# Performance work log

Measured on AMD Instinct MI355X. Metric: run time of the kernel, lower is better.

## Reference

```python
import jax, jax.numpy as jnp
from jax import lax
import numpy as np

B, N, C = 8, 10647, 80          # batch, total anchors (416px YOLOv3), COCO classes
MAX_BOXES = 100                  # yolo_max_boxes (per class and total, like combined NMS)
IOU_TH = 0.5
SCORE_TH = 0.3


def setup_inputs() -> dict:
    key = jax.random.key(0)
    k1, k2, k3, k4 = jax.random.split(key, 4)
    # valid corner-format boxes (x1,y1,x2,y2) in [0,1]
    xy = jax.random.uniform(k1, (B, N, 2), dtype=jnp.float32) * 0.9
    wh = jax.random.uniform(k2, (B, N, 2), dtype=jnp.float32) * 0.1 + 0.01
    boxes = jnp.concatenate([xy, xy + wh], axis=-1)
    confidence = jax.random.uniform(k3, (B, N, 1), dtype=jnp.float32)
    class_probs = jax.random.uniform(k4, (B, N, C), dtype=jnp.float32)
    return {"boxes": boxes, "confidence": confidence, "class_probs": class_probs}


def _iou_one_vs_all(box, boxes):
    # box [4], boxes [N,4], corner format
    x1 = jnp.maximum(box[0], boxes[:, 0])
    y1 = jnp.maximum(box[1], boxes[:, 1])
    x2 = jnp.minimum(box[2], boxes[:, 2])
    y2 = jnp.minimum(box[3], boxes[:, 3])
    inter = jnp.maximum(x2 - x1, 0.0) * jnp.maximum(y2 - y1, 0.0)
    area_a = (box[2] - box[0]) * (box[3] - box[1])
    area_b = (boxes[:, 2] - boxes[:, 0]) * (boxes[:, 3] - boxes[:, 1])
    return inter / (area_a + area_b - inter + 1e-9)


def _nms_one_class(scores_c, bxs):
    # scores_c [N], bxs [N,4]: greedy NMS, returns MAX_BOXES candidates
    s0 = jnp.where(scores_c > SCORE_TH, scores_c, -1.0)

    def step(cur, _):
        i = jnp.argmax(cur)
        sc = cur[i]
        b = bxs[i]
        ious = _iou_one_vs_all(b, bxs)
        nxt = jnp.where(ious > IOU_TH, -1.0, cur).at[i].set(-1.0)
        valid = sc > 0.0
        return nxt, (jnp.where(valid, sc, 0.0),
                     jnp.where(valid, b, jnp.zeros(4, b.dtype)),
                     valid)

    _, (ss, bb, vv) = lax.scan(step, s0, None, length=MAX_BOXES)
    return bb, ss, vv  # [M,4], [M], [M]


def reference(boxes, confidence, class_probs):
    # scores per class: objectness * class prob  -> [B, C, N]
    scores = jnp.transpose(confidence * class_probs, (0, 2, 1))
    per_class = jax.vmap(jax.vmap(_nms_one_class, in_axes=(0, None)), in_axes=(0, 0))
    cb, cs, cv = per_class(scores, boxes)           # [B,C,M,4], [B,C,M], [B,C,M]

    flat_s = cs.reshape(B, -1)                       # [B, C*M]
    flat_b = cb.reshape(B, -1, 4)
    flat_v = cv.reshape(B, -1)
    cls_ids = jnp.broadcast_to(
        jnp.arange(C, dtype=jnp.float32)[:, None], (C, MAX_BOXES)).reshape(-1)

    top_s, top_i = lax.top_k(flat_s, MAX_BOXES)      # merge across classes
    sel_b = jnp.take_along_axis(flat_b, top_i[..., None], axis=1)
    sel_v = jnp.take_along_axis(flat_v, top_i, axis=1)
    sel_c = jnp.where(sel_v, cls_ids[top_i], 0.0)
    sel_s = jnp.where(sel_v, top_s, 0.0)
    num_valid = jnp.sum(sel_v, axis=1).astype(jnp.int32)
    return sel_b, sel_s, sel_c, num_valid
```

## Files before the change

kernel.cpp:

```cpp
#include <hip/hip_runtime.h>

#define Bn 8
#define Nn 10647
#define Cn 80
#define MAXB 100
#define SCORE_TH 0.3f
#define BGUESS 0.82f
#define IOU_THR 0.5f
#define NBIN 4096
#define NB2 1024
#define SORT_CAP 256
#define TARGET 160
#define CH 128
#define PCAP 16
#define TOT (Cn * MAXB)
#define TOTQ (TOT / 4)
#define MREG 8

__device__ __forceinline__ int score_bin(float s) {
    int v = (int)(__float_as_uint(s) >> 12) - 0x3E999 + 1;
    v = v < 1 ? 1 : v;
    return v > NBIN - 1 ? NBIN - 1 : v;
}
__device__ __forceinline__ int score_bin2(float s) {
    int v = (int)(__float_as_uint(s) >> 14) - 0xFA66 + 1;
    v = v < 1 ? 1 : v;
    return v > NB2 - 1 ? NB2 - 1 : v;
}

__device__ __forceinline__ bool iou_gt(const float4 s, const float4 c) {
    float x1 = fmaxf(s.x, c.x), y1 = fmaxf(s.y, c.y);
    float x2 = fminf(s.z, c.z), y2 = fminf(s.w, c.w);
    float inter = fmaxf(x2 - x1, 0.0f) * fmaxf(y2 - y1, 0.0f);
    float aS = (s.z - s.x) * (s.w - s.y);
    float aC = (c.z - c.x) * (c.w - c.y);
    return inter > IOU_THR * (aS + aC - inter + 1e-9f);
}

__global__ __launch_bounds__(256) void collect(
    const float* __restrict__ conf, const float* __restrict__ cp,
    int* __restrict__ pcnt, unsigned long long* __restrict__ glist)
{
    __shared__ float lconf[88];
    __shared__ int cnt3[Cn];
    __shared__ int cnt9[Cn];
    int tid = threadIdx.x;
    int b = blockIdx.x / CH;
    int ch = blockIdx.x % CH;

    for (int i = tid; i < Cn; i += 256) { cnt3[i] = 0; cnt9[i] = 0; }

    const int totq = Nn * 20;
    const int per = (totq + CH - 1) / CH;
    int q0 = ch * per;
    int q1 = q0 + per; if (q1 > totq) q1 = totq;
    int n0 = q0 / 20;
    int nspan = (q1 - 1) / 20 - n0 + 1;

    const float* confB = conf + b * Nn;
    for (int i = tid; i < nspan; i += 256) lconf[i] = confB[n0 + i];
    __syncthreads();

    const float4* cp4 = (const float4*)(cp + (size_t)b * Nn * Cn);

    for (int q = q0 + tid; q < q1; q += 256) {
        float4 v = cp4[q];
        int n = q / 20;
        int c0 = (q % 20) * 4;
        float cf = lconf[n - n0];
        float sv[4] = {v.x, v.y, v.z, v.w};
#pragma unroll
        for (int e = 0; e < 4; ++e) {
            float s = cf * sv[e];
            if (s > SCORE_TH) {
                atomicAdd(&cnt3[c0 + e], 1);
                if (s > BGUESS) {
                    int pos = atomicAdd(&cnt9[c0 + e], 1);
                    if (pos < PCAP)
                        glist[((size_t)(b * Cn + c0 + e) * CH + ch) * PCAP + pos] =
                            ((unsigned long long)__float_as_uint(s) << 32) |
                            (unsigned)(Nn - 1 - n);
                }
            }
        }
    }
    __syncthreads();
    for (int c = tid; c < Cn; c += 256)
        pcnt[(size_t)(b * Cn + c) * CH + ch] = (cnt3[c] & 0xFFFF) | (cnt9[c] << 16);
}

__global__ __launch_bounds__(512) void nms_class(
    const float* __restrict__ boxes, const float* __restrict__ conf,
    const float* __restrict__ cp,
    const int* __restrict__ pcnt, const unsigned long long* __restrict__ glist,
    float* __restrict__ wss, float4* __restrict__ wsb)
{
    __shared__ unsigned long long keys[SORT_CAP];
    __shared__ float ssc[SORT_CAP];
    __shared__ float4 sbx[SORT_CAP];
    __shared__ float4 bxu[SORT_CAP];
    __shared__ unsigned short cj[SORT_CAP][3];
    __shared__ int ncA[SORT_CAP];
    __shared__ unsigned char selv[SORT_CAP], resv[SORT_CAP], confl[SORT_CAP];
    __shared__ int rpart[SORT_CAP];
    __shared__ int chc[CH], chOff[CH], pscan[CH];
    __shared__ int hist2[NB2];
    __shared__ int suf[257];
    __shared__ int wtot[4];
    __shared__ int sh_tot, sh_ovf, sh_hard, sh_B, sh_M, sh_nsel;

    int tid = threadIdx.x;
    int lane = tid & 63, wv = tid >> 6;
    int bc = blockIdx.x;
    int b = bc / Cn, c = bc % Cn;

    if (tid == 0) { sh_tot = 0; sh_ovf = 0; sh_hard = 0; sh_nsel = 0; }
    for (int i = tid; i < SORT_CAP; i += 512) ncA[i] = 0;
    __syncthreads();

    if (tid < CH) {
        int p = pcnt[(size_t)(b * Cn + c) * CH + tid];
        int c9 = p >> 16;
        if (c9 > PCAP) { atomicOr(&sh_ovf, 1); c9 = PCAP; }
        chc[tid] = c9;
        atomicAdd(&sh_tot, p & 0xFFFF);
        int incl = c9;
#pragma unroll
        for (int off = 1; off < 64; off <<= 1) {
            int o = __shfl_up(incl, off);
            if (lane >= off) incl += o;
        }
        pscan[tid] = incl;
    }
    float* ws_s = wss + bc * MAXB;
    float4* ws_b = wsb + bc * MAXB;
    for (int i = tid; i < MAXB; i += 512) ws_s[i] = 0.0f;
    __syncthreads();
    if (tid < CH) {
        int base = (tid >= 64) ? pscan[63] : 0;
        chOff[tid] = base + pscan[tid] - chc[tid];
    }
    __syncthreads();

    int cnt = pscan[63] + pscan[127];
    int tot = sh_tot;
    bool fast = (!sh_ovf) && (cnt <= SORT_CAP);
    int M = fast ? cnt : 0;

    if (fast) {
        const unsigned long long* slotC = glist + (size_t)(b * Cn + c) * CH * PCAP;
        for (int i = tid; i < CH * PCAP; i += 512) {
            int ch = i >> 4, j = i & (PCAP - 1);
            if (j < chc[ch]) keys[chOff[ch] + j] = slotC[i];
        }
    }
    __syncthreads();

    const float4* boxesB = (const float4*)boxes + (size_t)b * Nn;
    int cand = tid & 255, half = tid >> 8;
    bool act = (cand < M);

    unsigned long long k0 = 0;
    float4 b0 = make_float4(0, 0, 0, 0);
    if (act) k0 = keys[cand];
    if (act && half == 0) b0 = boxesB[Nn - 1 - (int)(k0 & 0xffffffffu)];
    int r0 = 0;
    if (act) {
#pragma unroll 4
        for (int j = half; j < M; j += 2) r0 += (keys[j] > k0) ? 1 : 0;
    }
    if (act && half == 1) rpart[cand] = r0;
    __syncthreads();
    if (act && half == 0) {
        int rank = r0 + rpart[cand];
        ssc[rank] = __uint_as_float((unsigned)(k0 >> 32));
        sbx[rank] = b0;
    }
    __syncthreads();

    if (act) {
        float4 tb = sbx[cand];
#pragma unroll 2
        for (int j = half; j < cand; j += 2) {
            float4 bj = sbx[j];
            if (iou_gt(bj, tb)) {
                int s = atomicAdd(&ncA[cand], 1);
                if (s < 3) cj[cand][s] = (unsigned short)j;
            }
        }
    }
    __syncthreads();
    if (tid < SORT_CAP && tid < M && ncA[tid] > 3) atomicOr(&sh_hard, 1);
    __syncthreads();

    if (!sh_hard) {
        bool mysel = false, myres = false;
        if (tid < SORT_CAP) {
            myres = (tid < M) ? (ncA[tid] == 0) : true;
            mysel = (tid < M) && myres;
            selv[tid] = mysel ? 1 : 0;
            resv[tid] = myres ? 1 : 0;
        }
        __syncthreads();
        while (true) {
            bool upd = false, upd_sel = false;
            if (tid < SORT_CAP && tid < M && !myres) {
                int nc = ncA[tid];
                bool allr = true, anysel = false;
                for (int k = 0; k < nc; ++k) {
                    int j = cj[tid][k];
                    allr = allr && (resv[j] != 0);
                    anysel = anysel || (selv[j] != 0);
                }
                if (allr) { upd = true; upd_sel = !anysel; }
            }
            __syncthreads();
            if (upd) {
                myres = true; mysel = upd_sel;
                selv[tid] = mysel ? 1 : 0; resv[tid] = 1;
            }
            int unres = __syncthreads_count((tid < SORT_CAP && tid < M && !myres) ? 1 : 0);
            if (unres == 0) break;
        }
        int v = (tid < SORT_CAP && mysel) ? 1 : 0;
        int incl = v;
        if (tid < SORT_CAP) {
#pragma unroll
            for (int off = 1; off < 64; off <<= 1) {
                int o = __shfl_up(incl, off);
                if (lane >= off) incl += o;
            }
            if (lane == 63) wtot[wv] = incl;
        }
        __syncthreads();
        if (tid < SORT_CAP) {
            int base = 0;
            for (int w = 0; w < wv; ++w) base += wtot[w];
            int pos = base + incl - v;
            if (v && pos < MAXB) { ws_s[pos] = ssc[tid]; ws_b[pos] = sbx[tid]; }
            if (tid == 0) sh_nsel = wtot[0] + wtot[1] + wtot[2] + wtot[3];
        }
        __syncthreads();
    } else {
        if (tid < SORT_CAP) confl[tid] = (tid < M && ncA[tid] > 0) ? 1 : 0;
        __syncthreads();
        if (tid < 64) {
            float4 sA = make_float4(0, 0, 0, 0), sB = make_float4(0, 0, 0, 0);
            int nsel = 0;
            for (int w0 = 0; w0 < M && nsel < MAXB; w0 += 64) {
                int wlim = M - w0; if (wlim > 64) wlim = 64;
                bool cfl = (tid < wlim) ? (confl[w0 + tid] != 0) : false;
                unsigned long long cmask = __ballot(cfl);
                int pos = 0;
                while (pos < wlim && nsel < MAXB) {
                    if (!((cmask >> pos) & 1ULL)) {
                        unsigned long long rest = cmask >> pos;
                        int run = rest ? (__ffsll(rest) - 1) : (wlim - pos);
                        if (run > wlim - pos) run = wlim - pos;
                        int avail = MAXB - nsel; if (run > avail) run = avail;
                        int d = (tid - (nsel & 63)) & 63;
                        if (d < run) {
                            int s = nsel + d;
                            int ci = w0 + pos + d;
                            float4 bx = sbx[ci];
                            if (s < 64) sA = bx; else sB = bx;
                            ws_s[s] = ssc[ci]; ws_b[s] = bx;
                        }
                        nsel += run; pos += run;
                    } else {
                        int ci = w0 + pos;
                        float4 bx = sbx[ci];
                        bool sup = (tid < nsel) && iou_gt(sA, bx);
                        if (tid + 64 < nsel) sup = sup || iou_gt(sB, bx);
                        if (__ballot(sup) == 0ULL) {
                            if (tid == (nsel & 63)) { if (nsel < 64) sA = bx; else sB = bx; }
                            if (tid == 0) { ws_s[nsel] = ssc[ci]; ws_b[nsel] = bx; }
                            ++nsel;
                        }
                        ++pos;
                    }
                }
            }
            if (tid == 0) sh_nsel = nsel;
        }
        __syncthreads();
    }

    bool needSlow = (!fast) || !((sh_nsel >= MAXB) || (cnt == tot));
    if (!needSlow) return;

    for (int i = tid; i < MAXB; i += 512) ws_s[i] = 0.0f;
    for (int i = tid; i < NB2; i += 512) hist2[i] = 0;
    if (tid == 0) sh_nsel = 0;
    __syncthreads();

    const float* confB = conf + b * Nn;
    const float* cpB = cp + (size_t)b * Nn * Cn + c;
    for (int n = tid; n < Nn; n += 512) {
        float s = confB[n] * cpB[(size_t)n * Cn];
        if (s > SCORE_TH) atomicAdd(&hist2[score_bin2(s)], 1);
    }
    __syncthreads();

    float4 sA = make_float4(0, 0, 0, 0), sB = make_float4(0, 0, 0, 0);
    int hi = NB2;
    int round = 0;

    while (true) {
        if (tid < 256) {
            int ps = 0;
#pragma unroll
            for (int u = 0; u < 4; ++u) ps += hist2[tid * 4 + u];
            int p = ps;
#pragma unroll
            for (int off = 1; off < 64; off <<= 1) {
                int v = __shfl_down(p, off);
                if (lane + off < 64) p += v;
            }
            if (lane == 0) wtot[wv] = p;
        }
        __syncthreads();
        if (tid < 256) {
            int add = 0;
            for (int w2 = wv + 1; w2 < 4; ++w2) add += wtot[w2];
            suf[tid] = ((tid < 256) ? 0 : 0) + add + ((lane < 64) ? 0 : 0);
        }
        __syncthreads();
        if (tid < 256) {
            int ps = 0;
#pragma unroll
            for (int u = 0; u < 4; ++u) ps += hist2[tid * 4 + u];
            int p = ps;
#pragma unroll
            for (int off = 1; off < 64; off <<= 1) {
                int v = __shfl_down(p, off);
                if (lane + off < 64) p += v;
            }
            int add = 0;
            for (int w2 = wv + 1; w2 < 4; ++w2) add += wtot[w2];
            suf[tid] = p + add;
            if (tid == 0) suf[256] = 0;
        }
        __syncthreads();

        int total = suf[0];
        if (total == 0) break;

        int target = total < TARGET ? total : TARGET;
        if (tid < 256 && suf[tid] >= target && suf[tid + 1] < target) sh_B = tid;
        if (tid == 0) sh_M = 0;
        __syncthreads();
        if (tid == 0) {
            int g = sh_B;
            int running = suf[g + 1];
            int B = g * 4;
            for (int u = 3; u >= 0; --u) {
                running += hist2[g * 4 + u];
                if (running >= target) { B = g * 4 + u; break; }
            }
            sh_B = B;
        }
        __syncthreads();
        int B = sh_B;

        for (int n = tid; n < Nn; n += 512) {
            float s = confB[n] * cpB[(size_t)n * Cn];
            if (s > SCORE_TH) {
                int bin = score_bin2(s);
                if (bin >= B && bin < hi) {
                    int pos2 = atomicAdd(&sh_M, 1);
                    if (pos2 < SORT_CAP)
                        keys[pos2] = ((unsigned long long)__float_as_uint(s) << 32) |
                                     (unsigned)(Nn - 1 - n);
                }
            }
        }
        __syncthreads();
        int M2 = sh_M; if (M2 > SORT_CAP) M2 = SORT_CAP;

        unsigned long long mk = 0;
        float4 mb = make_float4(0, 0, 0, 0);
        if (tid < 256) {
            if (tid < M2) { mk = keys[tid]; mb = boxesB[Nn - 1 - (int)(mk & 0xffffffffu)]; }
            bxu[tid] = mb;
        }
        __syncthreads();

        if (tid < 256) {
            int rank = 0;
            bool cfl = (round > 0);
            for (int j = 0; j < M2; ++j) {
                unsigned long long kk = keys[j];
                float4 bj = bxu[j];
                bool gt = kk > mk;
                rank += gt ? 1 : 0;
                if (round == 0) cfl = cfl || (gt && iou_gt(bj, mb));
            }
            if (tid < M2) {
                ssc[rank] = __uint_as_float((unsigned)(mk >> 32));
                sbx[rank] = mb; confl[rank] = cfl ? 1 : 0;
            }
        }
        __syncthreads();

        if (tid < 64) {
            int nsel = sh_nsel;
            for (int w0 = 0; w0 < M2 && nsel < MAXB; w0 += 64) {
                int wlim = M2 - w0; if (wlim > 64) wlim = 64;
                bool cfl2 = (tid < wlim) ? (confl[w0 + tid] != 0) : false;
                unsigned long long cmask = __ballot(cfl2);
                int pos = 0;
                while (pos < wlim && nsel < MAXB) {
                    if (!((cmask >> pos) & 1ULL)) {
                        unsigned long long rest = cmask >> pos;
                        int run = rest ? (__ffsll(rest) - 1) : (wlim - pos);
                        if (run > wlim - pos) run = wlim - pos;
                        int avail = MAXB - nsel; if (run > avail) run = avail;
                        int d = (tid - (nsel & 63)) & 63;
                        if (d < run) {
                            int s = nsel + d;
                            int ci = w0 + pos + d;
                            float4 bx = sbx[ci];
                            if (s < 64) sA = bx; else sB = bx;
                            ws_s[s] = ssc[ci]; ws_b[s] = bx;
                        }
                        nsel += run; pos += run;
                    } else {
                        int ci = w0 + pos;
                        float4 bx = sbx[ci];
                        bool sup = (tid < nsel) && iou_gt(sA, bx);
                        if (tid + 64 < nsel) sup = sup || iou_gt(sB, bx);
                        if (__ballot(sup) == 0ULL) {
                            if (tid == (nsel & 63)) { if (nsel < 64) sA = bx; else sB = bx; }
                            if (tid == 0) { ws_s[nsel] = ssc[ci]; ws_b[nsel] = bx; }
                            ++nsel;
                        }
                        ++pos;
                    }
                }
            }
            if (tid == 0) sh_nsel = nsel;
        }
        __syncthreads();
        if (sh_nsel >= MAXB) break;
        for (int i = B + tid; i < NB2; i += 512) hist2[i] = 0;
        hi = B;
        ++round;
        __syncthreads();
    }
}

__global__ __launch_bounds__(256) void merge_topk(
    const float* __restrict__ wss, const float4* __restrict__ wsb,
    float* __restrict__ out)
{
    __shared__ int hist[NBIN];
    __shared__ int suf[257];
    __shared__ int wtot[4];
    __shared__ unsigned long long keys[SORT_CAP];
    __shared__ unsigned long long skeys[SORT_CAP];
    __shared__ int sh_B, sh_M;

    int tid = threadIdx.x, b = blockIdx.x;
    int lane = tid & 63, wv = tid >> 6;
    for (int i = tid; i < NBIN / 4; i += 256) ((int4*)hist)[i] = make_int4(0, 0, 0, 0);
    if (tid == 0) sh_M = 0;
    skeys[tid] = 0ULL;
    __syncthreads();

    const float4* w4 = (const float4*)(wss + b * TOT);
    float4 rr[MREG];
#pragma unroll
    for (int k = 0; k < MREG; ++k) {
        int q = tid + k * 256;
        rr[k] = (q < TOTQ) ? w4[q] : make_float4(0, 0, 0, 0);
    }
#pragma unroll
    for (int k = 0; k < MREG; ++k) {
        float4 v = rr[k];
        if (v.x > 0.0f) atomicAdd(&hist[score_bin(v.x)], 1);
        if (v.y > 0.0f) atomicAdd(&hist[score_bin(v.y)], 1);
        if (v.z > 0.0f) atomicAdd(&hist[score_bin(v.z)], 1);
        if (v.w > 0.0f) atomicAdd(&hist[score_bin(v.w)], 1);
    }
    __syncthreads();

    int ps = 0;
#pragma unroll
    for (int u = 0; u < 16; ++u) ps += hist[tid * 16 + u];
    int p = ps;
#pragma unroll
    for (int off = 1; off < 64; off <<= 1) {
        int v = __shfl_down(p, off);
        if (lane + off < 64) p += v;
    }
    if (lane == 0) wtot[wv] = p;
    __syncthreads();
    int add = 0;
    for (int w2 = wv + 1; w2 < 4; ++w2) add += wtot[w2];
    suf[tid] = p + add;
    if (tid == 0) suf[256] = 0;
    __syncthreads();

    int total = suf[0];
    int target = total < MAXB ? total : MAXB;

    if (total > 0) {
        if (suf[tid] >= target && suf[tid + 1] < target) sh_B = tid;
    }
    __syncthreads();
    if (total > 0 && tid == 0) {
        int g = sh_B;
        int running = suf[g + 1];
        int B = g * 16;
        for (int u = 15; u >= 0; --u) {
            running += hist[g * 16 + u];
            if (running >= target) { B = g * 16 + u; break; }
        }
        sh_B = B;
    }
    __syncthreads();
    if (total > 0) {
        int B = sh_B;
#pragma unroll
        for (int k = 0; k < MREG; ++k) {
            int q = tid + k * 256;
            if (q < TOTQ) {
                float4 v = rr[k];
                int ib = q * 4;
                float sv[4] = {v.x, v.y, v.z, v.w};
#pragma unroll
                for (int e = 0; e < 4; ++e) {
                    float s = sv[e];
                    if (s > 0.0f && score_bin(s) >= B) {
                        int pos = atomicAdd(&sh_M, 1);
                        if (pos < SORT_CAP)
                            keys[pos] = ((unsigned long long)__float_as_uint(s) << 32) |
                                        (unsigned)(TOT - 1 - (ib + e));
                    }
                }
            }
        }
    }
    __syncthreads();
    int M = sh_M; if (M > SORT_CAP) M = SORT_CAP;

    unsigned long long mykey = (tid < M) ? keys[tid] : 0ULL;
    int rank = 0;
    for (int j = 0; j < M; ++j) rank += (keys[j] > mykey) ? 1 : 0;
    if (tid < M) skeys[rank] = mykey;
    __syncthreads();

    bool valid = false;
    if (tid < MAXB) {
        unsigned long long g = skeys[tid];
        valid = (g != 0ULL);
        float s = valid ? __uint_as_float((unsigned)(g >> 32)) : 0.0f;
        int f = TOT - 1 - (int)(g & 0xffffffffu);
        float4 bx = make_float4(0, 0, 0, 0);
        float cls = 0.0f;
        if (valid) { bx = wsb[b * TOT + f]; cls = (float)(f / MAXB); }
        ((float4*)out)[b * MAXB + tid] = bx;
        out[Bn * MAXB * 4 + b * MAXB + tid] = s;
        out[Bn * MAXB * 5 + b * MAXB + tid] = cls;
    }
    int nv = __syncthreads_count(valid);
    if (tid == 0) out[Bn * MAXB * 6 + b] = (float)nv;
}

extern "C" void kernel_launch(void* const* d_in, const int* in_sizes, int n_in,
                              void* d_out, int out_size, void* d_ws, size_t ws_size,
                              hipStream_t stream) {
    const float* boxes = (const float*)d_in[0];
    const float* conf  = (const float*)d_in[1];
    const float* cp    = (const float*)d_in[2];
    float* out = (float*)d_out;

    char* ws = (char*)d_ws;
    int* pcnt = (int*)(ws + 0);
    unsigned long long* glist = (unsigned long long*)(ws + 327680);
    size_t offWss = 327680 + (size_t)Bn * Cn * CH * PCAP * 8;
    float* wss = (float*)(ws + offWss);
    size_t offWsb = offWss + (size_t)640 * MAXB * 4;
    float4* wsb = (float4*)(ws + offWsb);

    collect<<<Bn * CH, 256, 0, stream>>>(conf, cp, pcnt, glist);
    nms_class<<<Bn * Cn, 512, 0, stream>>>(boxes, conf, cp, pcnt, glist, wss, wsb);
    merge_topk<<<Bn, 256, 0, stream>>>(wss, wsb, out);
}
```

Baseline: 50.65 us.

## Stage candidate boxes in collect, unroll loads, simplify suffix scan

The collect kernel now writes each high-score candidate's box next to its key in workspace. nms_class then reads boxes contiguously instead of gathering them from the full box array by anchor index. Collect also issues two float4 loads per iteration to raise memory-level parallelism, and the total count becomes a wave reduction instead of a shared atomic. The slow-path histogram suffix scan drops a redundant recompute pass. The trade is more workspace writes and a larger shared footprint (bxc).

```diff
diff --git a/kernel.cpp b/kernel.cpp
--- a/kernel.cpp
+++ b/kernel.cpp
@@ -39,7 +39,9 @@
 
 __global__ __launch_bounds__(256) void collect(
     const float* __restrict__ conf, const float* __restrict__ cp,
-    int* __restrict__ pcnt, unsigned long long* __restrict__ glist)
+    const float4* __restrict__ boxes,
+    int* __restrict__ pcnt, unsigned long long* __restrict__ gkey,
+    float4* __restrict__ gbox)
 {
     __shared__ float lconf[88];
     __shared__ int cnt3[Cn];
@@ -62,24 +64,36 @@
     __syncthreads();
 
     const float4* cp4 = (const float4*)(cp + (size_t)b * Nn * Cn);
-
-    for (int q = q0 + tid; q < q1; q += 256) {
-        float4 v = cp4[q];
-        int n = q / 20;
-        int c0 = (q % 20) * 4;
-        float cf = lconf[n - n0];
-        float sv[4] = {v.x, v.y, v.z, v.w};
-#pragma unroll
-        for (int e = 0; e < 4; ++e) {
-            float s = cf * sv[e];
-            if (s > SCORE_TH) {
-                atomicAdd(&cnt3[c0 + e], 1);
-                if (s > BGUESS) {
-                    int pos = atomicAdd(&cnt9[c0 + e], 1);
-                    if (pos < PCAP)
-                        glist[((size_t)(b * Cn + c0 + e) * CH + ch) * PCAP + pos] =
-                            ((unsigned long long)__float_as_uint(s) << 32) |
-                            (unsigned)(Nn - 1 - n);
+    const float4* boxesB = boxes + (size_t)b * Nn;
+
+    for (int q = q0 + tid; q < q1; q += 512) {
+        int qb = q + 256;
+        bool has2 = qb < q1;
+        float4 v1 = cp4[q];
+        float4 v2 = has2 ? cp4[qb] : make_float4(0, 0, 0, 0);
+#pragma unroll
+        for (int h = 0; h < 2; ++h) {
+            if (h == 1 && !has2) break;
+            int qq = (h == 0) ? q : qb;
+            float4 v = (h == 0) ? v1 : v2;
+            int n = qq / 20;
+            int c0 = (qq % 20) * 4;
+            float cf = lconf[n - n0];
+            float sv[4] = {v.x, v.y, v.z, v.w};
+#pragma unroll
+            for (int e = 0; e < 4; ++e) {
+                float s = cf * sv[e];
+                if (s > SCORE_TH) {
+                    atomicAdd(&cnt3[c0 + e], 1);
+                    if (s > BGUESS) {
+                        int pos = atomicAdd(&cnt9[c0 + e], 1);
+                        if (pos < PCAP) {
+                            size_t idx = ((size_t)(b * Cn + c0 + e) * CH + ch) * PCAP + pos;
+                            gkey[idx] = ((unsigned long long)__float_as_uint(s) << 32) |
+                                        (unsigned)(Nn - 1 - n);
+                            gbox[idx] = boxesB[n];
+                        }
+                    }
                 }
             }
         }
@@ -90,12 +104,14 @@
 }
 
 __global__ __launch_bounds__(512) void nms_class(
-    const float* __restrict__ boxes, const float* __restrict__ conf,
+    const float4* __restrict__ boxes, const float* __restrict__ conf,
     const float* __restrict__ cp,
-    const int* __restrict__ pcnt, const unsigned long long* __restrict__ glist,
+    const int* __restrict__ pcnt, const unsigned long long* __restrict__ gkey,
+    const float4* __restrict__ gbox,
     float* __restrict__ wss, float4* __restrict__ wsb)
 {
     __shared__ unsigned long long keys[SORT_CAP];
+    __shared__ float4 bxc[SORT_CAP];
     __shared__ float ssc[SORT_CAP];
     __shared__ float4 sbx[SORT_CAP];
     __shared__ float4 bxu[SORT_CAP];
@@ -107,14 +123,14 @@
     __shared__ int hist2[NB2];
     __shared__ int suf[257];
     __shared__ int wtot[4];
-    __shared__ int sh_tot, sh_ovf, sh_hard, sh_B, sh_M, sh_nsel;
+    __shared__ int sh_ovf, sh_hard, sh_B, sh_M, sh_nsel;
 
     int tid = threadIdx.x;
     int lane = tid & 63, wv = tid >> 6;
     int bc = blockIdx.x;
     int b = bc / Cn, c = bc % Cn;
 
-    if (tid == 0) { sh_tot = 0; sh_ovf = 0; sh_hard = 0; sh_nsel = 0; }
+    if (tid == 0) { sh_ovf = 0; sh_hard = 0; sh_nsel = 0; }
     for (int i = tid; i < SORT_CAP; i += 512) ncA[i] = 0;
     __syncthreads();
 
@@ -123,7 +139,6 @@
         int c9 = p >> 16;
         if (c9 > PCAP) { atomicOr(&sh_ovf, 1); c9 = PCAP; }
         chc[tid] = c9;
-        atomicAdd(&sh_tot, p & 0xFFFF);
         int incl = c9;
 #pragma unroll
         for (int off = 1; off < 64; off <<= 1) {
@@ -131,6 +146,10 @@
             if (lane >= off) incl += o;
         }
         pscan[tid] = incl;
+        int t3 = p & 0xFFFF;
+#pragma unroll
+        for (int off = 32; off > 0; off >>= 1) t3 += __shfl_down(t3, off);
+        if (lane == 0) wtot[wv] = t3;
     }
     float* ws_s = wss + bc * MAXB;
     float4* ws_b = wsb + bc * MAXB;
@@ -143,27 +162,30 @@
     __syncthreads();
 
     int cnt = pscan[63] + pscan[127];
-    int tot = sh_tot;
+    int tot = wtot[0] + wtot[1];
     bool fast = (!sh_ovf) && (cnt <= SORT_CAP);
     int M = fast ? cnt : 0;
 
     if (fast) {
-        const unsigned long long* slotC = glist + (size_t)(b * Cn + c) * CH * PCAP;
+        size_t base = (size_t)(b * Cn + c) * CH * PCAP;
         for (int i = tid; i < CH * PCAP; i += 512) {
             int ch = i >> 4, j = i & (PCAP - 1);
-            if (j < chc[ch]) keys[chOff[ch] + j] = slotC[i];
-        }
-    }
-    __syncthreads();
-
-    const float4* boxesB = (const float4*)boxes + (size_t)b * Nn;
+            if (j < chc[ch]) {
+                int dst = chOff[ch] + j;
+                keys[dst] = gkey[base + i];
+                bxc[dst] = gbox[base + i];
+            }
+        }
+    }
+    __syncthreads();
+
     int cand = tid & 255, half = tid >> 8;
     bool act = (cand < M);
 
     unsigned long long k0 = 0;
     float4 b0 = make_float4(0, 0, 0, 0);
     if (act) k0 = keys[cand];
-    if (act && half == 0) b0 = boxesB[Nn - 1 - (int)(k0 & 0xffffffffu)];
+    if (act && half == 0) b0 = bxc[cand];
     int r0 = 0;
     if (act) {
 #pragma unroll 4
@@ -180,7 +202,7 @@
 
     if (act) {
         float4 tb = sbx[cand];
-#pragma unroll 2
+#pragma unroll 4
         for (int j = half; j < cand; j += 2) {
             float4 bj = sbx[j];
             if (iou_gt(bj, tb)) {
@@ -294,6 +316,7 @@
     if (tid == 0) sh_nsel = 0;
     __syncthreads();
 
+    const float4* boxesB = boxes + (size_t)b * Nn;
     const float* confB = conf + b * Nn;
     const float* cpB = cp + (size_t)b * Nn * Cn + c;
     for (int n = tid; n < Nn; n += 512) {
@@ -318,27 +341,14 @@
                 if (lane + off < 64) p += v;
             }
             if (lane == 0) wtot[wv] = p;
+            pscan[0] = p;
+            suf[tid] = p;
         }
         __syncthreads();
         if (tid < 256) {
             int add = 0;
             for (int w2 = wv + 1; w2 < 4; ++w2) add += wtot[w2];
-            suf[tid] = ((tid < 256) ? 0 : 0) + add + ((lane < 64) ? 0 : 0);
-        }
-        __syncthreads();
-        if (tid < 256) {
-            int ps = 0;
-#pragma unroll
-            for (int u = 0; u < 4; ++u) ps += hist2[tid * 4 + u];
-            int p = ps;
-#pragma unroll
-            for (int off = 1; off < 64; off <<= 1) {
-                int v = __shfl_down(p, off);
-                if (lane + off < 64) p += v;
-            }
-            int add = 0;
-            for (int w2 = wv + 1; w2 < 4; ++w2) add += wtot[w2];
-            suf[tid] = p + add;
+            suf[tid] = suf[tid] + add;
             if (tid == 0) suf[256] = 0;
         }
         __syncthreads();
@@ -571,20 +581,20 @@
 extern "C" void kernel_launch(void* const* d_in, const int* in_sizes, int n_in,
                               void* d_out, int out_size, void* d_ws, size_t ws_size,
                               hipStream_t stream) {
-    const float* boxes = (const float*)d_in[0];
-    const float* conf  = (const float*)d_in[1];
-    const float* cp    = (const float*)d_in[2];
+    const float4* boxes = (const float4*)d_in[0];
+    const float* conf   = (const float*)d_in[1];
+    const float* cp     = (const float*)d_in[2];
     float* out = (float*)d_out;
 
     char* ws = (char*)d_ws;
     int* pcnt = (int*)(ws + 0);
-    unsigned long long* glist = (unsigned long long*)(ws + 327680);
-    size_t offWss = 327680 + (size_t)Bn * Cn * CH * PCAP * 8;
-    float* wss = (float*)(ws + offWss);
-    size_t offWsb = offWss + (size_t)640 * MAXB * 4;
-    float4* wsb = (float4*)(ws + offWsb);
-
-    collect<<<Bn * CH, 256, 0, stream>>>(conf, cp, pcnt, glist);
-    nms_class<<<Bn * Cn, 512, 0, stream>>>(boxes, conf, cp, pcnt, glist, wss, wsb);
+    unsigned long long* gkey = (unsigned long long*)(ws + 327680);
+    float4* gbox = (float4*)(ws + 10813440);
+    float* wss = (float*)(ws + 31784960);
+    float4* wsb = (float4*)(ws + 32040960);
+
+    collect<<<Bn * CH, 256, 0, stream>>>(conf, cp, boxes, pcnt, gkey, gbox);
+    nms_class<<<Bn * Cn, 512, 0, stream>>>(boxes, conf, cp, pcnt, gkey, gbox,
+                                           wss, wsb);
     merge_topk<<<Bn, 256, 0, stream>>>(wss, wsb, out);
 }
```

After: 53.65 us. +5.9%, slower.
